# Kernel optimization log

Hardware: AMD Instinct MI355X
Metric: run time of the kernel (lower is better)

Reference implementation:

```python
import jax, jax.numpy as jnp
import numpy as np

B, S, H = 1, 2048, 1024
NH, HD = 16, 64
WIN = 512
M_MEM, M_PER = 512, 64
SCALE = 1.0 / np.sqrt(HD)
NEG_INF = jnp.float32(-1e30)


def setup_inputs() -> dict:
    key = jax.random.key(0)
    ks = jax.random.split(key, 22)
    std = 1.0 / np.sqrt(H)
    def w(k):
        return (jax.random.normal(k, (H, H), jnp.float32) * std)
    names = ['local_wq','local_wk','local_wv','local_wo',
             'long_wq','long_wk','long_wv','long_wo',
             'mem_wq','mem_wk','mem_wv','mem_wo',
             'per_wq','per_wk','per_wv','per_wo']
    d = {n: w(ks[i]) for i, n in enumerate(names)}
    d['gate_w'] = jax.random.normal(ks[16], (4 * H, 4), jnp.float32) * 0.02
    d['gate_b'] = jnp.zeros((4,), jnp.float32)
    d['x'] = jax.random.normal(ks[17], (B, S, H), jnp.float32)
    d['memory_kv'] = jax.random.normal(ks[18], (B, M_MEM, H), jnp.float32)
    d['persona_kv'] = jax.random.normal(ks[19], (B, M_PER, H), jnp.float32)
    return d


def _split_heads(t):
    # (B, T, H) -> (B, NH, T, HD)
    b, t_, _ = t.shape
    return t.reshape(b, t_, NH, HD).transpose(0, 2, 1, 3)


def _merge_heads(t):
    b, h, t_, d = t.shape
    return t.transpose(0, 2, 1, 3).reshape(b, t_, h * d)


def _self_attn(x, wq, wk, wv, wo, mask):
    # mask: (S, S) bool, True = masked out
    q = _split_heads(x @ wq)
    k = _split_heads(x @ wk)
    v = _split_heads(x @ wv)
    scores = jnp.einsum('bhsd,bhtd->bhst', q, k) * SCALE
    scores = jnp.where(mask[None, None], NEG_INF, scores)
    a = jax.nn.softmax(scores, axis=-1)
    out = jnp.einsum('bhst,bhtd->bhsd', a, v)
    return _merge_heads(out) @ wo


def _cross_attn(x, ctx, wq, wk, wv, wo):
    q = _split_heads(x @ wq)
    k = _split_heads(ctx @ wk)
    v = _split_heads(ctx @ wv)
    scores = jnp.einsum('bhsd,bhmd->bhsm', q, k) * SCALE
    a = jax.nn.softmax(scores, axis=-1)
    out = jnp.einsum('bhsm,bhmd->bhsd', a, v)
    return _merge_heads(out) @ wo


def reference(x, memory_kv, persona_kv,
              local_wq, local_wk, local_wv, local_wo,
              long_wq, long_wk, long_wv, long_wo,
              mem_wq, mem_wk, mem_wv, mem_wo,
              per_wq, per_wk, per_wv, per_wo,
              gate_w, gate_b):
    s = x.shape[1]
    idx = jnp.arange(s)
    causal = idx[None, :] > idx[:, None]                    # future tokens masked
    local = causal | ((idx[:, None] - idx[None, :]) > WIN)  # sliding window + causal

    local_out = _self_attn(x, local_wq, local_wk, local_wv, local_wo, local)
    long_out = _self_attn(x, long_wq, long_wk, long_wv, long_wo, causal)
    mem_out = _cross_attn(x, memory_kv, mem_wq, mem_wk, mem_wv, mem_wo)
    per_out = _cross_attn(x, persona_kv, per_wq, per_wk, per_wv, per_wo)

    outs = (local_out, long_out, mem_out, per_out)
    gate_in = jnp.concatenate(outs, axis=-1)                # (B, S, 4H)
    gates = jax.nn.softmax(gate_in @ gate_w + gate_b, axis=-1)  # (B, S, 4)
    fused = sum(gates[..., i:i + 1] * o for i, o in enumerate(outs))
    return fused  # emotion_scale = 1.0, dropout off (eval)
```

## Files before the change

### kernel.cpp

```cpp
#include <hip/hip_runtime.h>

#define S 2048
#define H 1024
#define NH 16
#define HD 64
#define WIN 512
#define SCALE 0.125f

typedef unsigned short u16;
typedef __attribute__((ext_vector_type(8))) short bfrag;
typedef __attribute__((ext_vector_type(4))) float facc;
typedef __attribute__((ext_vector_type(4))) unsigned short u16x4;

constexpr size_t M1   = 1u << 20;
constexpr size_t WTO  = 0;
constexpr size_t XBO  = 8 * M1;
constexpr size_t MEMBO= 10 * M1;
constexpr size_t PERBO= MEMBO + (M1 >> 1);
constexpr size_t QO   = PERBO + (M1 >> 4);
constexpr size_t KVO  = QO + 8 * M1;
constexpr size_t K2O  = KVO + 8 * M1;
constexpr size_t V2O  = K2O + (M1 >> 1);
constexpr size_t K3O  = V2O + (M1 >> 1);
constexpr size_t V3O  = K3O + (M1 >> 4);

__device__ __forceinline__ u16 f2bf(float f) {
    union { float f; unsigned u; } v; v.f = f;
    unsigned r = v.u + 0x7fffu + ((v.u >> 16) & 1u);
    return (u16)(r >> 16);
}
__device__ __forceinline__ float bf2f(u16 b) {
    union { unsigned u; float f; } v; v.u = ((unsigned)b) << 16;
    return v.f;
}

__global__ __launch_bounds__(256)
void cast_bf16(const float* __restrict__ in, u16* __restrict__ out, int n8) {
    int i = blockIdx.x * 256 + threadIdx.x;
    if (i >= n8) return;
    const float4* p = reinterpret_cast<const float4*>(in) + (size_t)i * 2;
    float4 a = p[0], b = p[1];
    u16x4 o0, o1;
    o0[0] = f2bf(a.x); o0[1] = f2bf(a.y); o0[2] = f2bf(a.z); o0[3] = f2bf(a.w);
    o1[0] = f2bf(b.x); o1[1] = f2bf(b.y); o1[2] = f2bf(b.z); o1[3] = f2bf(b.w);
    u16x4* q = reinterpret_cast<u16x4*>(out) + (size_t)i * 2;
    q[0] = o0; q[1] = o1;
}

__global__ __launch_bounds__(256)
void transp_cast(const float* __restrict__ w0, const float* __restrict__ w1,
                 const float* __restrict__ w2, const float* __restrict__ w3,
                 u16* __restrict__ wt) {
    __shared__ float t[64][65];
    const float* w = blockIdx.z == 0 ? w0 : blockIdx.z == 1 ? w1
                   : blockIdx.z == 2 ? w2 : w3;
    u16* o = wt + (size_t)blockIdx.z * (1024 * 1024);
    const int kt = blockIdx.y * 64, nt = blockIdx.x * 64;
    const int r = threadIdx.x >> 4, c4 = (threadIdx.x & 15) * 4;
#pragma unroll
    for (int p = 0; p < 4; p++) {
        float4 v = *reinterpret_cast<const float4*>(
            &w[(size_t)(kt + r + p * 16) * 1024 + nt + c4]);
        t[r + p * 16][c4 + 0] = v.x; t[r + p * 16][c4 + 1] = v.y;
        t[r + p * 16][c4 + 2] = v.z; t[r + p * 16][c4 + 3] = v.w;
    }
    __syncthreads();
#pragma unroll
    for (int p = 0; p < 4; p++) {
        int nn = r + p * 16;
        u16x4 ov;
        ov[0] = f2bf(t[c4 + 0][nn]); ov[1] = f2bf(t[c4 + 1][nn]);
        ov[2] = f2bf(t[c4 + 2][nn]); ov[3] = f2bf(t[c4 + 3][nn]);
        *reinterpret_cast<u16x4*>(&o[(size_t)(nt + nn) * 1024 + kt + c4]) = ov;
    }
}

__global__ __launch_bounds__(256)
void gemm_bf16(const u16* __restrict__ A, const u16* __restrict__ Bt,
               u16* __restrict__ C, int M, long sA, long sB, long sC,
               int scaleMask) {
    __shared__ __align__(16) u16 sa[128 * 64];
    __shared__ __align__(16) u16 sb[128 * 64];
    A  += (size_t)blockIdx.z * sA;
    Bt += (size_t)blockIdx.z * sB;
    C  += (size_t)blockIdx.z * sC;
    const float scl = ((scaleMask >> blockIdx.z) & 1) ? SCALE : 1.0f;
    const int tid = threadIdx.x;
    const int wid = tid >> 6, lane = tid & 63;
    const int lhi = lane >> 4, llo = lane & 15;
    const int wm = wid >> 1, wn = wid & 1;
    const int row0 = blockIdx.y * 128, col0 = blockIdx.x * 128;

    facc acc[4][4];
#pragma unroll
    for (int i = 0; i < 4; i++)
#pragma unroll
        for (int j = 0; j < 4; j++)
#pragma unroll
            for (int k = 0; k < 4; k++) acc[i][j][k] = 0.f;

    int arow[4];
#pragma unroll
    for (int j = 0; j < 4; j++) {
        int r = (j * 256 + tid) >> 3;
        int ar = row0 + r; if (ar > M - 1) ar = M - 1;
        arow[j] = ar;
    }
    bfrag ra[4], rb[4];
    auto load_tile = [&](int k0) {
#pragma unroll
        for (int j = 0; j < 4; j++) {
            int idx = j * 256 + tid;
            int c = idx & 7, r = idx >> 3;
            ra[j] = *reinterpret_cast<const bfrag*>(&A[(size_t)arow[j] * 1024 + k0 + c * 8]);
            rb[j] = *reinterpret_cast<const bfrag*>(&Bt[(size_t)(col0 + r) * 1024 + k0 + c * 8]);
        }
    };
    load_tile(0);
    for (int kt = 0; kt < 16; kt++) {
        __syncthreads();
#pragma unroll
        for (int j = 0; j < 4; j++) {
            int idx = j * 256 + tid;
            int c = idx & 7, r = idx >> 3;
            int p = c ^ (r & 7);
            *reinterpret_cast<bfrag*>(&sa[r * 64 + p * 8]) = ra[j];
            *reinterpret_cast<bfrag*>(&sb[r * 64 + p * 8]) = rb[j];
        }
        __syncthreads();
        if (kt < 15) load_tile((kt + 1) * 64);
#pragma unroll
        for (int ks = 0; ks < 2; ks++) {
            bfrag af[4], bfv[4];
#pragma unroll
            for (int mf = 0; mf < 4; mf++) {
                int r = wm * 64 + mf * 16 + llo;
                int p = (ks * 4 + lhi) ^ (r & 7);
                af[mf] = *reinterpret_cast<const bfrag*>(&sa[r * 64 + p * 8]);
            }
#pragma unroll
            for (int nf = 0; nf < 4; nf++) {
                int r = wn * 64 + nf * 16 + llo;
                int p = (ks * 4 + lhi) ^ (r & 7);
                bfv[nf] = *reinterpret_cast<const bfrag*>(&sb[r * 64 + p * 8]);
            }
            __builtin_amdgcn_s_setprio(1);
#pragma unroll
            for (int mf = 0; mf < 4; mf++)
#pragma unroll
                for (int nf = 0; nf < 4; nf++)
                    acc[mf][nf] = __builtin_amdgcn_mfma_f32_16x16x32_bf16(
                        af[mf], bfv[nf], acc[mf][nf], 0, 0, 0);
            __builtin_amdgcn_s_setprio(0);
        }
    }
#pragma unroll
    for (int mf = 0; mf < 4; mf++) {
#pragma unroll
        for (int r = 0; r < 4; r++) {
            int row = row0 + wm * 64 + mf * 16 + lhi * 4 + r;
            if (row < M) {
#pragma unroll
                for (int nf = 0; nf < 4; nf++) {
                    int col = col0 + wn * 64 + nf * 16 + llo;
                    C[(size_t)row * 1024 + col] = f2bf(acc[mf][nf][r] * scl);
                }
            }
        }
    }
}

__global__ __launch_bounds__(256)
void attn_merged(u16* __restrict__ ws) {
    __shared__ __align__(16) u16 ksm[64 * 64];
    __shared__ __align__(16) u16 vtm[64 * 64];
    __shared__ __align__(16) u16 psm[4 * 16 * 64];

    int blk = blockIdx.x;
    int branch, h, qt;
    if (blk < 512)       { branch = 1; qt = 31 - (blk >> 4); h = blk & 15; }
    else if (blk < 1024) { int t = blk - 512;  branch = 0; qt = 31 - (t >> 4); h = t & 15; }
    else if (blk < 1536) { int t = blk - 1024; branch = 2; qt = t >> 4; h = t & 15; }
    else                 { int t = blk - 1536; branch = 3; qt = t >> 4; h = t & 15; }

    size_t kb, vb; int Skv, mask;
    if (branch == 0)      { kb = KVO;          vb = KVO + 2 * M1; Skv = 2048; mask = 2; }
    else if (branch == 1) { kb = KVO + 4 * M1; vb = KVO + 6 * M1; Skv = 2048; mask = 1; }
    else if (branch == 2) { kb = K2O;          vb = V2O;          Skv = 512;  mask = 0; }
    else                  { kb = K3O;          vb = V3O;          Skv = 64;   mask = 0; }
    const u16* Kp = ws + kb;
    const u16* Vp = ws + vb;
    u16* Qp = ws + QO + (size_t)branch * 2 * M1;

    const int tid = threadIdx.x, wid = tid >> 6, lane = tid & 63;
    const int lhi = lane >> 4, llo = lane & 15;
    const int q0 = qt * 64;
    const int hoff = h * 64;

    bfrag qf[2];
    {
        const u16* qp = &Qp[(size_t)(q0 + wid * 16 + llo) * 1024 + hoff + lhi * 8];
        qf[0] = *reinterpret_cast<const bfrag*>(qp);
        qf[1] = *reinterpret_cast<const bfrag*>(qp + 32);
    }
    facc acc_o[4];
    float m_r[4], l_r[4];
#pragma unroll
    for (int r = 0; r < 4; r++) { m_r[r] = -1e30f; l_r[r] = 0.f; }
#pragma unroll
    for (int nf = 0; nf < 4; nf++)
#pragma unroll
        for (int k = 0; k < 4; k++) acc_o[nf][k] = 0.f;

    const int ktEnd = (mask >= 1) ? (qt + 1) : (Skv >> 6);
    const int ktBeg = (mask == 2 && q0 >= WIN) ? ((q0 - WIN) >> 6) : 0;
    const int vkey = tid & 63, vdb = (tid >> 6) * 16;

    bfrag rk[2], rv[2];
    auto load_kv = [&](int kt) {
#pragma unroll
        for (int j = 0; j < 2; j++) {
            int idx = j * 256 + tid;
            int key = idx >> 3, c = idx & 7;
            rk[j] = *reinterpret_cast<const bfrag*>(
                &Kp[(size_t)(kt * 64 + key) * 1024 + hoff + c * 8]);
        }
        const u16* vp = &Vp[(size_t)(kt * 64 + vkey) * 1024 + hoff + vdb];
        rv[0] = *reinterpret_cast<const bfrag*>(vp);
        rv[1] = *reinterpret_cast<const bfrag*>(vp + 8);
    };
    load_kv(ktBeg);

    for (int kt = ktBeg; kt < ktEnd; kt++) {
        __syncthreads();
#pragma unroll
        for (int j = 0; j < 2; j++) {
            int idx = j * 256 + tid;
            int key = idx >> 3, c = idx & 7;
            *reinterpret_cast<bfrag*>(&ksm[key * 64 + (c ^ (key & 7)) * 8]) = rk[j];
        }
        {
            int kc = vkey >> 3, kp = vkey & 7;
#pragma unroll
            for (int j = 0; j < 2; j++)
#pragma unroll
                for (int i = 0; i < 8; i++) {
                    int d = vdb + j * 8 + i;
                    vtm[d * 64 + ((kc ^ (d & 7)) * 8 + kp)] = (u16)(unsigned short)rv[j][i];
                }
        }
        __syncthreads();
        if (kt + 1 < ktEnd) load_kv(kt + 1);

        facc sc[4];
#pragma unroll
        for (int nf = 0; nf < 4; nf++)
#pragma unroll
            for (int k = 0; k < 4; k++) sc[nf][k] = 0.f;
        __builtin_amdgcn_s_setprio(1);
#pragma unroll
        for (int nf = 0; nf < 4; nf++) {
#pragma unroll
            for (int ks = 0; ks < 2; ks++) {
                int r = nf * 16 + llo;
                int p = (ks * 4 + lhi) ^ (r & 7);
                bfrag kf = *reinterpret_cast<const bfrag*>(&ksm[r * 64 + p * 8]);
                sc[nf] = __builtin_amdgcn_mfma_f32_16x16x32_bf16(qf[ks], kf, sc[nf], 0, 0, 0);
            }
        }
        __builtin_amdgcn_s_setprio(0);
        float s[4][4];
#pragma unroll
        for (int nf = 0; nf < 4; nf++)
#pragma unroll
            for (int r = 0; r < 4; r++) s[nf][r] = sc[nf][r];

        const bool diag = (mask >= 1) && (kt == qt);
        const bool wedge = (mask == 2) && (q0 >= WIN) && (kt == ktBeg);
        if (diag || wedge) {
#pragma unroll
            for (int nf = 0; nf < 4; nf++)
#pragma unroll
                for (int r = 0; r < 4; r++) {
                    int key = kt * 64 + nf * 16 + llo;
                    int qi = q0 + wid * 16 + lhi * 4 + r;
                    if ((diag && key > qi) || (wedge && (qi - key) > WIN))
                        s[nf][r] = -1e30f;
                }
        }
        float alpha[4];
#pragma unroll
        for (int r = 0; r < 4; r++) {
            float mx = fmaxf(fmaxf(s[0][r], s[1][r]), fmaxf(s[2][r], s[3][r]));
            mx = fmaxf(mx, __shfl_xor(mx, 1));
            mx = fmaxf(mx, __shfl_xor(mx, 2));
            mx = fmaxf(mx, __shfl_xor(mx, 4));
            mx = fmaxf(mx, __shfl_xor(mx, 8));
            float mn = fmaxf(m_r[r], mx);
            alpha[r] = __expf(m_r[r] - mn);
            m_r[r] = mn;
            float rs = 0.f;
#pragma unroll
            for (int nf = 0; nf < 4; nf++) {
                float pv = __expf(s[nf][r] - mn);
                s[nf][r] = pv; rs += pv;
            }
            rs += __shfl_xor(rs, 1);
            rs += __shfl_xor(rs, 2);
            rs += __shfl_xor(rs, 4);
            rs += __shfl_xor(rs, 8);
            l_r[r] = l_r[r] * alpha[r] + rs;
        }
#pragma unroll
        for (int nf = 0; nf < 4; nf++)
#pragma unroll
            for (int r = 0; r < 4; r++) acc_o[nf][r] *= alpha[r];

        u16* pw = &psm[wid * 1024];
#pragma unroll
        for (int nf = 0; nf < 4; nf++) {
            int kc = nf * 2 + (llo >> 3), kp = llo & 7;
#pragma unroll
            for (int r = 0; r < 4; r++) {
                int row = lhi * 4 + r;
                pw[row * 64 + ((kc ^ (row & 7)) * 8 + kp)] = f2bf(s[nf][r]);
            }
        }
        __builtin_amdgcn_s_setprio(1);
#pragma unroll
        for (int ks = 0; ks < 2; ks++) {
            int pp = (ks * 4 + lhi) ^ (llo & 7);
            bfrag pf = *reinterpret_cast<const bfrag*>(&pw[llo * 64 + pp * 8]);
#pragma unroll
            for (int nf = 0; nf < 4; nf++) {
                int d = nf * 16 + llo;
                int vp2 = (ks * 4 + lhi) ^ (d & 7);
                bfrag vf = *reinterpret_cast<const bfrag*>(&vtm[d * 64 + vp2 * 8]);
                acc_o[nf] = __builtin_amdgcn_mfma_f32_16x16x32_bf16(pf, vf, acc_o[nf], 0, 0, 0);
            }
        }
        __builtin_amdgcn_s_setprio(0);
    }
#pragma unroll
    for (int r = 0; r < 4; r++) {
        float inv = 1.f / l_r[r];
#pragma unroll
        for (int nf = 0; nf < 4; nf++) {
            int row = q0 + wid * 16 + lhi * 4 + r;
            int col = hoff + nf * 16 + llo;
            Qp[(size_t)row * 1024 + col] = f2bf(acc_o[nf][r] * inv);
        }
    }
}

__global__ __launch_bounds__(256)
void gate_fuse(const u16* __restrict__ o4, const float* __restrict__ gw,
               const float* __restrict__ gb, float* __restrict__ out) {
    const size_t SHsz = (size_t)S * H;
    const int s = blockIdx.x, tid = threadIdx.x;
    const u16* ob0 = o4 + (size_t)s * H;
    float p[4] = {0.f, 0.f, 0.f, 0.f};
    for (int b = 0; b < 4; b++) {
        const u16* obb = ob0 + b * 2 * M1;
        const float* gwb = gw + (size_t)b * H * 4;
        for (int i = tid; i < H; i += 256) {
            float xv = bf2f(obb[i]);
            float4 g4 = *reinterpret_cast<const float4*>(&gwb[(size_t)i * 4]);
            p[0] += xv * g4.x; p[1] += xv * g4.y;
            p[2] += xv * g4.z; p[3] += xv * g4.w;
        }
    }
#pragma unroll
    for (int off = 1; off < 64; off <<= 1)
#pragma unroll
        for (int j = 0; j < 4; j++) p[j] += __shfl_xor(p[j], off);
    __shared__ float red[4][4];
    if ((tid & 63) == 0) {
        int w = tid >> 6;
#pragma unroll
        for (int j = 0; j < 4; j++) red[w][j] = p[j];
    }
    __syncthreads();
    float gl[4];
#pragma unroll
    for (int j = 0; j < 4; j++)
        gl[j] = gb[j] + red[0][j] + red[1][j] + red[2][j] + red[3][j];
    float mx = fmaxf(fmaxf(gl[0], gl[1]), fmaxf(gl[2], gl[3]));
    float e[4]; float tot = 0.f;
#pragma unroll
    for (int j = 0; j < 4; j++) { e[j] = __expf(gl[j] - mx); tot += e[j]; }
    float inv = 1.f / tot;
    int d = tid * 4;
    float4 rv; rv.x = rv.y = rv.z = rv.w = 0.f;
#pragma unroll
    for (int b = 0; b < 4; b++) {
        const u16* obb = ob0 + b * 2 * M1 + d;
        float wgt = e[b] * inv;
        rv.x += wgt * bf2f(obb[0]);
        rv.y += wgt * bf2f(obb[1]);
        rv.z += wgt * bf2f(obb[2]);
        rv.w += wgt * bf2f(obb[3]);
    }
    *reinterpret_cast<float4*>(&out[(size_t)s * H + d]) = rv;
}

extern "C" void kernel_launch(void* const* d_in, const int* in_sizes, int n_in,
                              void* d_out, int out_size, void* d_ws, size_t ws_size,
                              hipStream_t stream) {
    const float* Wm[16];
    for (int i = 0; i < 16; i++) Wm[i] = (const float*)d_in[i];
    const float* gw = (const float*)d_in[16];
    const float* gb = (const float*)d_in[17];
    const float* x = (const float*)d_in[18];
    const float* mem = (const float*)d_in[19];
    const float* per = (const float*)d_in[20];
    float* out = (float*)d_out;
    u16* ws = (u16*)d_ws;
    const size_t SH = (size_t)S * H;

    dim3 blk(256);
    cast_bf16<<<dim3(1024), blk, 0, stream>>>(x, ws + XBO, (int)(SH / 8));
    cast_bf16<<<dim3(256), blk, 0, stream>>>(mem, ws + MEMBO, 512 * 1024 / 8);
    cast_bf16<<<dim3(32), blk, 0, stream>>>(per, ws + PERBO, 64 * 1024 / 8);

    transp_cast<<<dim3(16, 16, 4), blk, 0, stream>>>(
        Wm[0], Wm[4], Wm[8], Wm[12], ws + WTO);
    transp_cast<<<dim3(16, 16, 4), blk, 0, stream>>>(
        Wm[1], Wm[2], Wm[5], Wm[6], ws + WTO + 4 * M1);
    gemm_bf16<<<dim3(8, 16, 8), blk, 0, stream>>>(
        ws + XBO, ws + WTO, ws + QO, 2048, 0, (long)M1, (long)(2 * M1), 0xF);

    transp_cast<<<dim3(16, 16, 4), blk, 0, stream>>>(
        Wm[9], Wm[10], Wm[13], Wm[14], ws + WTO);
    gemm_bf16<<<dim3(8, 4, 2), blk, 0, stream>>>(
        ws + MEMBO, ws + WTO, ws + K2O, 512, 0, (long)M1, (long)(M1 >> 1), 0);
    gemm_bf16<<<dim3(8, 1, 2), blk, 0, stream>>>(
        ws + PERBO, ws + WTO + 2 * M1, ws + K3O, 64, 0, (long)M1, (long)(M1 >> 4), 0);

    attn_merged<<<dim3(2048), blk, 0, stream>>>(ws);

    transp_cast<<<dim3(16, 16, 4), blk, 0, stream>>>(
        Wm[3], Wm[7], Wm[11], Wm[15], ws + WTO);
    gemm_bf16<<<dim3(8, 16, 4), blk, 0, stream>>>(
        ws + QO, ws + WTO, ws + KVO, 2048, (long)(2 * M1), (long)M1, (long)(2 * M1), 0);

    gate_fuse<<<dim3(S), blk, 0, stream>>>(ws + KVO, gw, gb, out);
}
```

Baseline: 204.3 us.

## Pre-transpose V and use single-wave swapped-operand attention without shared K/V staging

```diff
diff --git a/kernel.cpp b/kernel.cpp
--- a/kernel.cpp
+++ b/kernel.cpp
@@ -8,21 +8,25 @@
 #define SCALE 0.125f
 
 typedef unsigned short u16;
+typedef unsigned int u32;
 typedef __attribute__((ext_vector_type(8))) short bfrag;
 typedef __attribute__((ext_vector_type(4))) float facc;
 typedef __attribute__((ext_vector_type(4))) unsigned short u16x4;
 
-constexpr size_t M1   = 1u << 20;
-constexpr size_t WTO  = 0;
-constexpr size_t XBO  = 8 * M1;
-constexpr size_t MEMBO= 10 * M1;
-constexpr size_t PERBO= MEMBO + (M1 >> 1);
-constexpr size_t QO   = PERBO + (M1 >> 4);
-constexpr size_t KVO  = QO + 8 * M1;
-constexpr size_t K2O  = KVO + 8 * M1;
-constexpr size_t V2O  = K2O + (M1 >> 1);
-constexpr size_t K3O  = V2O + (M1 >> 1);
-constexpr size_t V3O  = K3O + (M1 >> 4);
+constexpr size_t M1    = 1u << 20;
+constexpr size_t WTO   = 0;
+constexpr size_t XBO   = 8 * M1;
+constexpr size_t MEMBO = 10 * M1;
+constexpr size_t PERBO = MEMBO + (M1 >> 1);
+constexpr size_t QO    = PERBO + (M1 >> 4);
+constexpr size_t KVO   = QO + 8 * M1;
+constexpr size_t K2O   = KVO + 8 * M1;
+constexpr size_t V2O   = K2O + (M1 >> 1);
+constexpr size_t K3O   = V2O + (M1 >> 1);
+constexpr size_t V3O   = K3O + (M1 >> 4);
+constexpr size_t VT1O  = V3O + (M1 >> 4);
+constexpr size_t VT2O  = VT1O + 2 * M1;
+constexpr size_t VT3O  = VT2O + (M1 >> 1);
 
 __device__ __forceinline__ u16 f2bf(float f) {
     union { float f; unsigned u; } v; v.f = f;
@@ -72,6 +76,43 @@
         ov[0] = f2bf(t[c4 + 0][nn]); ov[1] = f2bf(t[c4 + 1][nn]);
         ov[2] = f2bf(t[c4 + 2][nn]); ov[3] = f2bf(t[c4 + 3][nn]);
         *reinterpret_cast<u16x4*>(&o[(size_t)(nt + nn) * 1024 + kt + c4]) = ov;
+    }
+}
+
+__global__ __launch_bounds__(256)
+void transp_v(u16* __restrict__ ws) {
+    const int z = blockIdx.z;
+    const int Skv = (z < 2) ? 2048 : (z == 2 ? 512 : 64);
+    const int kb = blockIdx.x;
+    if (kb * 64 >= Skv) return;
+    const int h = blockIdx.y;
+    const u16* V = ws + (z == 0 ? KVO + 2 * M1 : z == 1 ? KVO + 6 * M1
+                       : z == 2 ? V2O : V3O);
+    u16* VT = ws + (z == 0 ? XBO : z == 1 ? VT1O : z == 2 ? VT2O : VT3O);
+    __shared__ __align__(16) u16 t[64][72];
+    {
+        const int r = threadIdx.x >> 3, c8 = (threadIdx.x & 7) * 8;
+#pragma unroll
+        for (int p = 0; p < 2; p++) {
+            int rr = r + p * 32;
+            bfrag v = *reinterpret_cast<const bfrag*>(
+                &V[(size_t)(kb * 64 + rr) * 1024 + h * 64 + c8]);
+            *reinterpret_cast<bfrag*>(&t[rr][c8]) = v;
+        }
+    }
+    __syncthreads();
+    {
+        const int d = threadIdx.x & 63;
+        const int k8b = (threadIdx.x >> 6) * 8;
+#pragma unroll
+        for (int p = 0; p < 2; p++) {
+            int k8 = k8b + p * 32;
+            bfrag o;
+#pragma unroll
+            for (int j = 0; j < 8; j++) o[j] = (short)t[k8 + j][d];
+            *reinterpret_cast<bfrag*>(
+                &VT[(size_t)(h * 64 + d) * Skv + kb * 64 + k8]) = o;
+        }
     }
 }
 
@@ -170,185 +211,163 @@
     }
 }
 
-__global__ __launch_bounds__(256)
-void attn_merged(u16* __restrict__ ws) {
-    __shared__ __align__(16) u16 ksm[64 * 64];
-    __shared__ __align__(16) u16 vtm[64 * 64];
-    __shared__ __align__(16) u16 psm[4 * 16 * 64];
-
-    int blk = blockIdx.x;
-    int branch, h, qt;
-    if (blk < 512)       { branch = 1; qt = 31 - (blk >> 4); h = blk & 15; }
-    else if (blk < 1024) { int t = blk - 512;  branch = 0; qt = 31 - (t >> 4); h = t & 15; }
-    else if (blk < 1536) { int t = blk - 1024; branch = 2; qt = t >> 4; h = t & 15; }
-    else                 { int t = blk - 1536; branch = 3; qt = t >> 4; h = t & 15; }
-
-    size_t kb, vb; int Skv, mask;
-    if (branch == 0)      { kb = KVO;          vb = KVO + 2 * M1; Skv = 2048; mask = 2; }
-    else if (branch == 1) { kb = KVO + 4 * M1; vb = KVO + 6 * M1; Skv = 2048; mask = 1; }
-    else if (branch == 2) { kb = K2O;          vb = V2O;          Skv = 512;  mask = 0; }
-    else                  { kb = K3O;          vb = V3O;          Skv = 64;   mask = 0; }
-    const u16* Kp = ws + kb;
-    const u16* Vp = ws + vb;
+__global__ __launch_bounds__(64, 2)
+void attn_swapped(u16* __restrict__ ws) {
+    __shared__ __align__(16) u16 psm[2][16][72];
+
+    const int blk = blockIdx.x;
+    int branch, h, qb;
+    if (blk < 1024)      { branch = 1; qb = 63 - (blk >> 4); h = blk & 15; }
+    else if (blk < 2048) { int t = blk - 1024; branch = 0; qb = 63 - (t >> 4); h = t & 15; }
+    else if (blk < 3072) { int t = blk - 2048; branch = 2; qb = t >> 4; h = t & 15; }
+    else                 { int t = blk - 3072; branch = 3; qb = t >> 4; h = t & 15; }
+
+    size_t kb_, vb_; int Skv, maskMode;
+    if (branch == 0)      { kb_ = KVO;          vb_ = XBO;  Skv = 2048; maskMode = 2; }
+    else if (branch == 1) { kb_ = KVO + 4 * M1; vb_ = VT1O; Skv = 2048; maskMode = 1; }
+    else if (branch == 2) { kb_ = K2O;          vb_ = VT2O; Skv = 512;  maskMode = 0; }
+    else                  { kb_ = K3O;          vb_ = VT3O; Skv = 64;   maskMode = 0; }
+    const u16* Kp  = ws + kb_;
+    const u16* VTp = ws + vb_;
     u16* Qp = ws + QO + (size_t)branch * 2 * M1;
 
-    const int tid = threadIdx.x, wid = tid >> 6, lane = tid & 63;
-    const int lhi = lane >> 4, llo = lane & 15;
-    const int q0 = qt * 64;
+    const int lane = threadIdx.x;
+    const int llo = lane & 15, lhi = lane >> 4;
+    const int q0 = qb * 32;
     const int hoff = h * 64;
 
-    bfrag qf[2];
-    {
-        const u16* qp = &Qp[(size_t)(q0 + wid * 16 + llo) * 1024 + hoff + lhi * 8];
-        qf[0] = *reinterpret_cast<const bfrag*>(qp);
-        qf[1] = *reinterpret_cast<const bfrag*>(qp + 32);
-    }
-    facc acc_o[4];
-    float m_r[4], l_r[4];
-#pragma unroll
-    for (int r = 0; r < 4; r++) { m_r[r] = -1e30f; l_r[r] = 0.f; }
-#pragma unroll
-    for (int nf = 0; nf < 4; nf++)
-#pragma unroll
-        for (int k = 0; k < 4; k++) acc_o[nf][k] = 0.f;
-
-    const int ktEnd = (mask >= 1) ? (qt + 1) : (Skv >> 6);
-    const int ktBeg = (mask == 2 && q0 >= WIN) ? ((q0 - WIN) >> 6) : 0;
-    const int vkey = tid & 63, vdb = (tid >> 6) * 16;
-
-    bfrag rk[2], rv[2];
-    auto load_kv = [&](int kt) {
-#pragma unroll
-        for (int j = 0; j < 2; j++) {
-            int idx = j * 256 + tid;
-            int key = idx >> 3, c = idx & 7;
-            rk[j] = *reinterpret_cast<const bfrag*>(
-                &Kp[(size_t)(kt * 64 + key) * 1024 + hoff + c * 8]);
-        }
-        const u16* vp = &Vp[(size_t)(kt * 64 + vkey) * 1024 + hoff + vdb];
-        rv[0] = *reinterpret_cast<const bfrag*>(vp);
-        rv[1] = *reinterpret_cast<const bfrag*>(vp + 8);
-    };
-    load_kv(ktBeg);
+    bfrag qf[2][2];
+#pragma unroll
+    for (int sub = 0; sub < 2; sub++)
+#pragma unroll
+        for (int ds = 0; ds < 2; ds++)
+            qf[sub][ds] = *reinterpret_cast<const bfrag*>(
+                &Qp[(size_t)(q0 + sub * 16 + llo) * 1024 + hoff + ds * 32 + lhi * 8]);
+
+    facc ot[2][4];
+    float mR[2], lR[2];
+#pragma unroll
+    for (int sub = 0; sub < 2; sub++) {
+        mR[sub] = -1e30f; lR[sub] = 0.f;
+#pragma unroll
+        for (int db = 0; db < 4; db++)
+#pragma unroll
+            for (int k = 0; k < 4; k++) ot[sub][db][k] = 0.f;
+    }
+
+    const int ktEnd = maskMode ? (q0 >> 6) + 1 : (Skv >> 6);
+    const int ktBeg = (maskMode == 2 && q0 >= WIN) ? ((q0 - WIN) >> 6) : 0;
+
+    const u16* kcol = Kp + (size_t)llo * 1024 + hoff + lhi * 8;
+    const u16* vcol = VTp + (size_t)(hoff + llo) * Skv + lhi * 8;
 
     for (int kt = ktBeg; kt < ktEnd; kt++) {
-        __syncthreads();
-#pragma unroll
-        for (int j = 0; j < 2; j++) {
-            int idx = j * 256 + tid;
-            int key = idx >> 3, c = idx & 7;
-            *reinterpret_cast<bfrag*>(&ksm[key * 64 + (c ^ (key & 7)) * 8]) = rk[j];
-        }
-        {
-            int kc = vkey >> 3, kp = vkey & 7;
-#pragma unroll
-            for (int j = 0; j < 2; j++)
-#pragma unroll
-                for (int i = 0; i < 8; i++) {
-                    int d = vdb + j * 8 + i;
-                    vtm[d * 64 + ((kc ^ (d & 7)) * 8 + kp)] = (u16)(unsigned short)rv[j][i];
+        bfrag kf[4][2], vf[4][2];
+#pragma unroll
+        for (int nf = 0; nf < 4; nf++)
+#pragma unroll
+            for (int ds = 0; ds < 2; ds++)
+                kf[nf][ds] = *reinterpret_cast<const bfrag*>(
+                    &kcol[(size_t)(kt * 64 + nf * 16) * 1024 + ds * 32]);
+#pragma unroll
+        for (int db = 0; db < 4; db++)
+#pragma unroll
+            for (int ks = 0; ks < 2; ks++)
+                vf[db][ks] = *reinterpret_cast<const bfrag*>(
+                    &vcol[(size_t)db * 16 * Skv + kt * 64 + ks * 32]);
+
+        const bool diag  = maskMode && (kt == (q0 >> 6));
+        const bool wedge = (maskMode == 2) && (kt == ktBeg) && (q0 >= WIN);
+
+#pragma unroll
+        for (int sub = 0; sub < 2; sub++) {
+            facc st[4];
+#pragma unroll
+            for (int nf = 0; nf < 4; nf++) {
+#pragma unroll
+                for (int k = 0; k < 4; k++) st[nf][k] = 0.f;
+            }
+            __builtin_amdgcn_s_setprio(1);
+#pragma unroll
+            for (int nf = 0; nf < 4; nf++)
+#pragma unroll
+                for (int ds = 0; ds < 2; ds++)
+                    st[nf] = __builtin_amdgcn_mfma_f32_16x16x32_bf16(
+                        kf[nf][ds], qf[sub][ds], st[nf], 0, 0, 0);
+            __builtin_amdgcn_s_setprio(0);
+
+            float s[16];
+#pragma unroll
+            for (int nf = 0; nf < 4; nf++)
+#pragma unroll
+                for (int r = 0; r < 4; r++) s[nf * 4 + r] = st[nf][r];
+
+            const int qi = q0 + sub * 16 + llo;
+            if (diag || wedge) {
+#pragma unroll
+                for (int nf = 0; nf < 4; nf++)
+#pragma unroll
+                    for (int r = 0; r < 4; r++) {
+                        int key = kt * 64 + nf * 16 + lhi * 4 + r;
+                        if ((diag && key > qi) ||
+                            (wedge && (qi - key) > WIN))
+                            s[nf * 4 + r] = -1e30f;
+                    }
+            }
+            float mx = s[0];
+#pragma unroll
+            for (int i = 1; i < 16; i++) mx = fmaxf(mx, s[i]);
+            mx = fmaxf(mx, __shfl_xor(mx, 16));
+            mx = fmaxf(mx, __shfl_xor(mx, 32));
+            float mn = fmaxf(mR[sub], mx);
+            float al = __expf(mR[sub] - mn);
+            mR[sub] = mn;
+            float sum = 0.f;
+#pragma unroll
+            for (int i = 0; i < 16; i++) {
+                float p = __expf(s[i] - mn);
+                s[i] = p; sum += p;
+            }
+            sum += __shfl_xor(sum, 16);
+            sum += __shfl_xor(sum, 32);
+            lR[sub] = lR[sub] * al + sum;
+#pragma unroll
+            for (int db = 0; db < 4; db++)
+#pragma unroll
+                for (int k = 0; k < 4; k++) ot[sub][db][k] *= al;
+
+#pragma unroll
+            for (int nf = 0; nf < 4; nf++)
+#pragma unroll
+                for (int rp = 0; rp < 2; rp++) {
+                    u32 w = (u32)f2bf(s[nf * 4 + rp * 2]) |
+                            ((u32)f2bf(s[nf * 4 + rp * 2 + 1]) << 16);
+                    *reinterpret_cast<u32*>(
+                        &psm[sub][llo][nf * 16 + lhi * 4 + rp * 2]) = w;
                 }
-        }
-        __syncthreads();
-        if (kt + 1 < ktEnd) load_kv(kt + 1);
-
-        facc sc[4];
-#pragma unroll
-        for (int nf = 0; nf < 4; nf++)
-#pragma unroll
-            for (int k = 0; k < 4; k++) sc[nf][k] = 0.f;
-        __builtin_amdgcn_s_setprio(1);
-#pragma unroll
-        for (int nf = 0; nf < 4; nf++) {
-#pragma unroll
-            for (int ks = 0; ks < 2; ks++) {
-                int r = nf * 16 + llo;
-                int p = (ks * 4 + lhi) ^ (r & 7);
-                bfrag kf = *reinterpret_cast<const bfrag*>(&ksm[r * 64 + p * 8]);
-                sc[nf] = __builtin_amdgcn_mfma_f32_16x16x32_bf16(qf[ks], kf, sc[nf], 0, 0, 0);
-            }
-        }
-        __builtin_amdgcn_s_setprio(0);
-        float s[4][4];
-#pragma unroll
-        for (int nf = 0; nf < 4; nf++)
-#pragma unroll
-            for (int r = 0; r < 4; r++) s[nf][r] = sc[nf][r];
-
-        const bool diag = (mask >= 1) && (kt == qt);
-        const bool wedge = (mask == 2) && (q0 >= WIN) && (kt == ktBeg);
-        if (diag || wedge) {
-#pragma unroll
-            for (int nf = 0; nf < 4; nf++)
-#pragma unroll
-                for (int r = 0; r < 4; r++) {
-                    int key = kt * 64 + nf * 16 + llo;
-                    int qi = q0 + wid * 16 + lhi * 4 + r;
-                    if ((diag && key > qi) || (wedge && (qi - key) > WIN))
-                        s[nf][r] = -1e30f;
-                }
-        }
-        float alpha[4];
-#pragma unroll
-        for (int r = 0; r < 4; r++) {
-            float mx = fmaxf(fmaxf(s[0][r], s[1][r]), fmaxf(s[2][r], s[3][r]));
-            mx = fmaxf(mx, __shfl_xor(mx, 1));
-            mx = fmaxf(mx, __shfl_xor(mx, 2));
-            mx = fmaxf(mx, __shfl_xor(mx, 4));
-            mx = fmaxf(mx, __shfl_xor(mx, 8));
-            float mn = fmaxf(m_r[r], mx);
-            alpha[r] = __expf(m_r[r] - mn);
-            m_r[r] = mn;
-            float rs = 0.f;
-#pragma unroll
-            for (int nf = 0; nf < 4; nf++) {
-                float pv = __expf(s[nf][r] - mn);
-                s[nf][r] = pv; rs += pv;
-            }
-            rs += __shfl_xor(rs, 1);
-            rs += __shfl_xor(rs, 2);
-            rs += __shfl_xor(rs, 4);
-            rs += __shfl_xor(rs, 8);
-            l_r[r] = l_r[r] * alpha[r] + rs;
-        }
-#pragma unroll
-        for (int nf = 0; nf < 4; nf++)
-#pragma unroll
-            for (int r = 0; r < 4; r++) acc_o[nf][r] *= alpha[r];
-
-        u16* pw = &psm[wid * 1024];
-#pragma unroll
-        for (int nf = 0; nf < 4; nf++) {
-            int kc = nf * 2 + (llo >> 3), kp = llo & 7;
-#pragma unroll
-            for (int r = 0; r < 4; r++) {
-                int row = lhi * 4 + r;
-                pw[row * 64 + ((kc ^ (row & 7)) * 8 + kp)] = f2bf(s[nf][r]);
-            }
-        }
-        __builtin_amdgcn_s_setprio(1);
-#pragma unroll
-        for (int ks = 0; ks < 2; ks++) {
-            int pp = (ks * 4 + lhi) ^ (llo & 7);
-            bfrag pf = *reinterpret_cast<const bfrag*>(&pw[llo * 64 + pp * 8]);
-#pragma unroll
-            for (int nf = 0; nf < 4; nf++) {
-                int d = nf * 16 + llo;
-                int vp2 = (ks * 4 + lhi) ^ (d & 7);
-                bfrag vf = *reinterpret_cast<const bfrag*>(&vtm[d * 64 + vp2 * 8]);
-                acc_o[nf] = __builtin_amdgcn_mfma_f32_16x16x32_bf16(pf, vf, acc_o[nf], 0, 0, 0);
-            }
-        }
-        __builtin_amdgcn_s_setprio(0);
-    }
-#pragma unroll
-    for (int r = 0; r < 4; r++) {
-        float inv = 1.f / l_r[r];
-#pragma unroll
-        for (int nf = 0; nf < 4; nf++) {
-            int row = q0 + wid * 16 + lhi * 4 + r;
-            int col = hoff + nf * 16 + llo;
-            Qp[(size_t)row * 1024 + col] = f2bf(acc_o[nf][r] * inv);
+            bfrag pf0 = *reinterpret_cast<const bfrag*>(&psm[sub][llo][lhi * 8]);
+            bfrag pf1 = *reinterpret_cast<const bfrag*>(&psm[sub][llo][32 + lhi * 8]);
+            __builtin_amdgcn_s_setprio(1);
+#pragma unroll
+            for (int db = 0; db < 4; db++) {
+                ot[sub][db] = __builtin_amdgcn_mfma_f32_16x16x32_bf16(
+                    vf[db][0], pf0, ot[sub][db], 0, 0, 0);
+                ot[sub][db] = __builtin_amdgcn_mfma_f32_16x16x32_bf16(
+                    vf[db][1], pf1, ot[sub][db], 0, 0, 0);
+            }
+            __builtin_amdgcn_s_setprio(0);
+        }
+    }
+#pragma unroll
+    for (int sub = 0; sub < 2; sub++) {
+        float inv = 1.f / lR[sub];
+        u16* orow = &Qp[(size_t)(q0 + sub * 16 + llo) * 1024 + hoff];
+#pragma unroll
+        for (int db = 0; db < 4; db++) {
+            u16x4 pk;
+#pragma unroll
+            for (int r = 0; r < 4; r++) pk[r] = f2bf(ot[sub][db][r] * inv);
+            *reinterpret_cast<u16x4*>(&orow[db * 16 + lhi * 4]) = pk;
         }
     }
 }
@@ -356,7 +375,6 @@
 __global__ __launch_bounds__(256)
 void gate_fuse(const u16* __restrict__ o4, const float* __restrict__ gw,
                const float* __restrict__ gb, float* __restrict__ out) {
-    const size_t SHsz = (size_t)S * H;
     const int s = blockIdx.x, tid = threadIdx.x;
     const u16* ob0 = o4 + (size_t)s * H;
     float p[4] = {0.f, 0.f, 0.f, 0.f};
@@ -437,12 +455,14 @@
     gemm_bf16<<<dim3(8, 1, 2), blk, 0, stream>>>(
         ws + PERBO, ws + WTO + 2 * M1, ws + K3O, 64, 0, (long)M1, (long)(M1 >> 4), 0);
 
-    attn_merged<<<dim3(2048), blk, 0, stream>>>(ws);
+    transp_v<<<dim3(32, 16, 4), blk, 0, stream>>>(ws);
+    attn_swapped<<<dim3(4096), dim3(64), 0, stream>>>(ws);
 
     transp_cast<<<dim3(16, 16, 4), blk, 0, stream>>>(
         Wm[3], Wm[7], Wm[11], Wm[15], ws + WTO);
     gemm_bf16<<<dim3(8, 16, 4), blk, 0, stream>>>(
-        ws + QO, ws + WTO, ws + KVO, 2048, (long)(2 * M1), (long)M1, (long)(2 * M1), 0);
+        ws + QO, ws + WTO, ws + KVO, 2048, (long)(2 * M1), (long)M1,
+        (long)(2 * M1), 0);
 
     gate_fuse<<<dim3(S), blk, 0, stream>>>(ws + KVO, gw, gb, out);
 }
```

Result: slower. 226.8 us (+11.0%).
